# Performance work log

Measured on AMD Instinct MI355X. Metric: run time of the kernel, lower is better.

## Reference

```python
import jax, jax.numpy as jnp
import numpy as np

L = 512       # seq_len (capped by hard-coded max_length=512)
LEN = 2048    # input feature dim ('length')
D = 2048      # d_model
H = 16        # num_heads
DH = D // H   # d_head = 128
FF = 8192     # FFN hidden
EPS = 1e-5


def _pos_encoding(n, d):
    # Matches PositionalEncoderLayer buffer construction exactly.
    pos = jnp.arange(n, dtype=jnp.float32)[:, None]                              # [n,1]
    freqs = 1.0 / (2.0 * jnp.pi) / (10000.0 * jnp.exp(jnp.arange(0, d, 2, dtype=jnp.float32) / d))
    pe = jnp.zeros((n, d), dtype=jnp.float32)
    pe = pe.at[:, 0::2].set(jnp.sin(2.0 * jnp.pi * freqs * pos))
    pe = pe.at[:, 1::2].set(jnp.cos(2.0 * jnp.pi * freqs * pos))
    return pe


def _layernorm(x, g, b):
    mu = jnp.mean(x, axis=-1, keepdims=True)
    var = jnp.mean((x - mu) ** 2, axis=-1, keepdims=True)
    return (x - mu) / jnp.sqrt(var + EPS) * g + b


def setup_inputs() -> dict:
    key = jax.random.key(0)
    ks = jax.random.split(key, 12)
    def lin(k, fin, fout):
        kw, kb = jax.random.split(k)
        W = jax.random.normal(kw, (fin, fout), jnp.float32) / np.sqrt(fin)
        b = jax.random.normal(kb, (fout,), jnp.float32) * 0.01
        return W, b
    emb_W, emb_b = lin(ks[0], LEN, D)
    Wq, bq = lin(ks[1], D, D)
    Wk, bk = lin(ks[2], D, D)
    Wv, bv = lin(ks[3], D, D)
    Wo, bo = lin(ks[4], D, D)
    W1, b1 = lin(ks[5], D, FF)
    W2, b2 = lin(ks[6], FF, D)
    return {
        "sequence": jax.random.normal(ks[7], (L, LEN), jnp.float32),
        "emb_W": emb_W, "emb_b": emb_b,
        "Wq": Wq, "bq": bq, "Wk": Wk, "bk": bk, "Wv": Wv, "bv": bv,
        "Wo": Wo, "bo": bo,
        "ln_g": jnp.ones((D,), jnp.float32), "ln_b": jnp.zeros((D,), jnp.float32),
        "W1": W1, "b1": b1, "W2": W2, "b2": b2,
    }


def reference(sequence, emb_W, emb_b, Wq, bq, Wk, bk, Wv, bv, Wo, bo, ln_g, ln_b, W1, b1, W2, b2):
    # Embedding + positional encoding
    X = sequence @ emb_W + emb_b                         # [L, D]
    X = X + _pos_encoding(X.shape[0], X.shape[1])
    # Multi-head attention (keeps the module's [L, d_head, H] layout)
    Q = (X @ Wq + bq).reshape(-1, DH, H)
    K = (X @ Wk + bk).reshape(-1, DH, H)
    V = (X @ Wv + bv).reshape(-1, DH, H)
    scores = jnp.einsum('ldh,mdh->lmh', Q, K) / jnp.sqrt(jnp.float32(D))  # [L, L, H]
    attn = jax.nn.softmax(scores, axis=1)                # softmax over keys
    A = jnp.einsum('lmh,mdh->ldh', attn, V).reshape(-1, D) @ Wo + bo
    # Residual + shared LayerNorm, FFN, residual + shared LayerNorm
    Xa = _layernorm(A + X, ln_g, ln_b)
    F = jax.nn.gelu(Xa @ W1 + b1) @ W2 + b2
    return _layernorm(F + Xa, ln_g, ln_b)
```

## Files before the change

kernel.cpp:

```cpp
#include <hip/hip_runtime.h>
#include <hip/hip_bf16.h>


typedef __bf16 bf16_t;
typedef __bf16 bf16x8 __attribute__((ext_vector_type(8)));
typedef float  f32x4  __attribute__((ext_vector_type(4)));

#define SEQL 512
#define DM   2048
#define FFH  8192
#define NH   16
#define DHD  128
#define PST  ((size_t)SEQL*DM)

__device__ __forceinline__ unsigned short bfbits(float f){
  bf16_t h = (bf16_t)f;
  return __builtin_bit_cast(unsigned short, h);
}
__device__ __forceinline__ unsigned int pack2(float a, float b){
  return (unsigned int)bfbits(a) | ((unsigned int)bfbits(b) << 16);
}

__device__ __forceinline__ void gll16(const bf16_t* g, bf16_t* l){
  __builtin_amdgcn_global_load_lds(
      (const __attribute__((address_space(1))) void*)g,
      (__attribute__((address_space(3))) void*)l, 16, 0, 0);
}

__global__ __launch_bounds__(256)
void cvt_bf16(const float* __restrict__ in, bf16_t* __restrict__ out){
  const int i = (blockIdx.x * 256 + threadIdx.x) * 4;
  const float4 v = *(const float4*)(in + i);
  ushort4 o;
  o.x = bfbits(v.x); o.y = bfbits(v.y); o.z = bfbits(v.z); o.w = bfbits(v.w);
  *(ushort4*)(out + i) = o;
}

constexpr int E_PART = 0;
constexpr int E_QKV  = 1;
constexpr int E_FFN1 = 2;

template<int EPI, int PERM>
__global__ __launch_bounds__(256, 4)
void gemmF(const bf16_t* __restrict__ A,
           const float* __restrict__ W0p, const float* __restrict__ W1p,
           const float* __restrict__ W2p,
           const float* __restrict__ b0p, const float* __restrict__ b1p,
           const float* __restrict__ b2p,
           float* __restrict__ outF, bf16_t* __restrict__ o0,
           bf16_t* __restrict__ o1, bf16_t* __restrict__ o2,
           int nn, int Nw, int K, int Kc)
{
  __shared__ bf16_t sA[2][64*32];
  __shared__ bf16_t sB[2][128*32];
  const int tid  = threadIdx.x;
  const int lane = tid & 63, w = tid >> 6;
  const int wr4 = w >> 1, wc = w & 1;
  const int c = lane & 15, g = lane >> 4;

  const int nwg = gridDim.x, cpx = nwg >> 3;
  const int sblk = (blockIdx.x & 7) * cpx + (blockIdx.x >> 3);
  const int mt = sblk & 7, q = sblk >> 3;
  const int nt = q % nn, zt = q / nn;
  const int m0 = mt * 64, k0 = zt * Kc;

  const float* Wp = W0p; int nb0 = nt * 128;
  if constexpr (EPI == E_QKV){
    if (nt >= 32){ Wp = W2p; nb0 = (nt - 32) * 128; }
    else if (nt >= 16){ Wp = W1p; nb0 = (nt - 16) * 128; }
  }

  const int sr = tid >> 2, ss = tid & 3;
  const int scol = ((ss ^ ((sr >> 1) & 3)) << 3);
  const bf16_t* Asrc = A + (size_t)(m0 + sr) * K + k0 + scol;

  const int bn4 = tid & 31;
  const int kb  = (tid >> 5) * 4;
  const float* Bsrc = Wp + nb0 + bn4 * 4;

  int raA[2], raB[4];
#pragma unroll
  for (int m = 0; m < 2; ++m){
    const int r = wr4*32 + m*16 + c;
    raA[m] = r*32 + ((g ^ ((r >> 1) & 3)) << 3);
  }
#pragma unroll
  for (int n = 0; n < 4; ++n){
    const int r = wc*64 + n*16 + c;
    raB[n] = r*32 + ((g ^ ((r >> 2) & 3)) << 3);
  }

  f32x4 wr[4];

#define LOADW(kt) {                                                         \
    const int kk = k0 + (kt)*32 + kb;                                       \
    _Pragma("unroll")                                                       \
    for (int i = 0; i < 4; ++i){                                            \
      const int kr = kk + i;                                                \
      const int krow = PERM ? (((kr & 127) << 4) + (kr >> 7)) : kr;         \
      wr[i] = *(const f32x4*)(Bsrc + (size_t)krow * Nw);                    \
    } }

#define STAGEA(bf, kt) gll16(Asrc + (size_t)(kt)*32, &sA[bf][tid*8]);

#define WRITEB(bf) {                                                        \
    _Pragma("unroll")                                                       \
    for (int j = 0; j < 4; ++j){                                            \
      const int n = bn4*4 + j;                                              \
      const int el = n*32 + (kb ^ (((n >> 2) & 3) << 3));                   \
      uint2 v2;                                                             \
      v2.x = pack2(wr[0][j], wr[1][j]);                                     \
      v2.y = pack2(wr[2][j], wr[3][j]);                                     \
      *(uint2*)&sB[bf][el] = v2;                                            \
    } }

  f32x4 acc[2][4] = {};
  const int nk = Kc >> 5;

  LOADW(0);
  STAGEA(0, 0);
  WRITEB(0);
  __syncthreads();

  int buf = 0;
  for (int kt = 0; kt < nk; ++kt){
    const int nb = buf ^ 1;
    if (kt + 1 < nk){ LOADW(kt + 1); STAGEA(nb, kt + 1); }
    bf16x8 af[2], bq4[4];
#pragma unroll
    for (int m = 0; m < 2; ++m) af[m] = *(const bf16x8*)&sA[buf][raA[m]];
#pragma unroll
    for (int n = 0; n < 4; ++n) bq4[n] = *(const bf16x8*)&sB[buf][raB[n]];
#pragma unroll
    for (int m = 0; m < 2; ++m)
#pragma unroll
      for (int n = 0; n < 4; ++n)
        acc[m][n] = __builtin_amdgcn_mfma_f32_16x16x32_bf16(af[m], bq4[n], acc[m][n], 0,0,0);
    if (kt + 1 < nk){ WRITEB(nb); }
    __syncthreads();
    buf = nb;
  }
#undef LOADW
#undef STAGEA
#undef WRITEB

#pragma unroll
  for (int n = 0; n < 4; ++n){
    const int col = nt*128 + wc*64 + n*16 + c;
#pragma unroll
    for (int m = 0; m < 2; ++m){
      const int row0 = m0 + wr4*32 + m*16 + 4*g;
      const f32x4 a4 = acc[m][n];
      if constexpr (EPI == E_PART){
        float* dst = outF + (size_t)zt * PST;
#pragma unroll
        for (int rr = 0; rr < 4; ++rr)
          dst[(size_t)(row0+rr)*DM + col] = a4[rr];
      } else if constexpr (EPI == E_QKV){
        if (col < DM){
          const float bv = b0p[col];
#pragma unroll
          for (int rr = 0; rr < 4; ++rr)
            o0[(size_t)(row0+rr)*DM + col] = (bf16_t)(a4[rr] + bv);
        } else if (col < 2*DM){
          const int cc = col - DM;
          const float bv = b1p[cc];
#pragma unroll
          for (int rr = 0; rr < 4; ++rr)
            o1[(size_t)(row0+rr)*DM + cc] = (bf16_t)(a4[rr] + bv);
        } else {
          const int cc = col - 2*DM;
          const float bv = b2p[cc];
          const int hh = cc & 15, dd = cc >> 4;
          unsigned short us[4];
#pragma unroll
          for (int rr = 0; rr < 4; ++rr) us[rr] = bfbits(a4[rr] + bv);
          *(ushort4*)&o2[(size_t)(hh*DHD + dd)*SEQL + row0] =
              make_ushort4(us[0], us[1], us[2], us[3]);
        }
      } else if constexpr (EPI == E_FFN1){
        const float bv = b0p[col];
#pragma unroll
        for (int rr = 0; rr < 4; ++rr){
          const float v = a4[rr] + bv;
          const float z = v * (v*v*0.044715f + 1.0f) * 1.5957691216f;
          const float gg = v / (1.0f + __expf(-z));
          o0[(size_t)(row0+rr)*FFH + col] = (bf16_t)gg;
        }
      }
    }
  }
}

__global__ __launch_bounds__(256)
void permute_qk(const bf16_t* __restrict__ Qf, const bf16_t* __restrict__ Kf,
                bf16_t* __restrict__ Qhd, bf16_t* __restrict__ Khd)
{
  const int row = blockIdx.x, which = blockIdx.y, tid = threadIdx.x;
  const bf16_t* src = (which ? Kf : Qf) + (size_t)row * DM;
  bf16_t* dst = which ? Khd : Qhd;
  const int hh = tid >> 4, d0 = (tid & 15) * 8;
  unsigned short us[8];
#pragma unroll
  for (int j = 0; j < 8; ++j)
    us[j] = __builtin_bit_cast(unsigned short, src[(d0 + j)*NH + hh]);
  uint4 o;
  o.x = (unsigned)us[0] | ((unsigned)us[1] << 16);
  o.y = (unsigned)us[2] | ((unsigned)us[3] << 16);
  o.z = (unsigned)us[4] | ((unsigned)us[5] << 16);
  o.w = (unsigned)us[6] | ((unsigned)us[7] << 16);
  *(uint4*)&dst[(size_t)hh*(SEQL*DHD) + (size_t)row*DHD + d0] = o;
}

__global__ __launch_bounds__(256)
void attn_kernel(const bf16_t* __restrict__ Qh, const bf16_t* __restrict__ Kh,
                 const bf16_t* __restrict__ Vt, bf16_t* __restrict__ Aout)
{
  __shared__ bf16_t Pl[32*512];
  __shared__ float redm[4][32];
  __shared__ float reds[4][32];
  const int tid = threadIdx.x;
  const int lane = tid & 63, w = tid >> 6;
  const int c = lane & 15, g = lane >> 4;
  const int h = blockIdx.y;
  const int rb = blockIdx.x * 32;
  const bf16_t* Qb = Qh + (size_t)h * (SEQL*DHD);
  const bf16_t* Kb = Kh + (size_t)h * (SEQL*DHD);
  const bf16_t* Vb = Vt + (size_t)h * (SEQL*DHD);

  bf16x8 qf[2][4];
#pragma unroll
  for (int a = 0; a < 2; ++a)
#pragma unroll
    for (int ks = 0; ks < 4; ++ks)
      qf[a][ks] = *(const bf16x8*)(Qb + (size_t)(rb + a*16 + c)*DHD + ks*32 + g*8);

  f32x4 s[2][8] = {};
#pragma unroll
  for (int ks = 0; ks < 4; ++ks)
#pragma unroll
    for (int b = 0; b < 8; ++b){
      const bf16x8 kf = *(const bf16x8*)(Kb + (size_t)(w*128 + b*16 + c)*DHD + ks*32 + g*8);
      s[0][b] = __builtin_amdgcn_mfma_f32_16x16x32_bf16(qf[0][ks], kf, s[0][b], 0,0,0);
      s[1][b] = __builtin_amdgcn_mfma_f32_16x16x32_bf16(qf[1][ks], kf, s[1][b], 0,0,0);
    }
#pragma unroll
  for (int a = 0; a < 2; ++a)
#pragma unroll
    for (int b = 0; b < 8; ++b)
#pragma unroll
      for (int rr = 0; rr < 4; ++rr) s[a][b][rr] *= 0.022097086912079612f;

  float mx[2][4], sm[2][4], inv[2][4];
#pragma unroll
  for (int a = 0; a < 2; ++a)
#pragma unroll
    for (int rr = 0; rr < 4; ++rr){
      float m = s[a][0][rr];
#pragma unroll
      for (int b = 1; b < 8; ++b) m = fmaxf(m, s[a][b][rr]);
#pragma unroll
      for (int off = 1; off < 16; off <<= 1) m = fmaxf(m, __shfl_xor(m, off));
      mx[a][rr] = m;
    }
  if (c == 0)
#pragma unroll
    for (int a = 0; a < 2; ++a)
#pragma unroll
      for (int rr = 0; rr < 4; ++rr) redm[w][a*16 + 4*g + rr] = mx[a][rr];
  __syncthreads();
#pragma unroll
  for (int a = 0; a < 2; ++a)
#pragma unroll
    for (int rr = 0; rr < 4; ++rr){
      const int lr = a*16 + 4*g + rr;
      mx[a][rr] = fmaxf(fmaxf(redm[0][lr], redm[1][lr]), fmaxf(redm[2][lr], redm[3][lr]));
      sm[a][rr] = 0.f;
    }
#pragma unroll
  for (int a = 0; a < 2; ++a)
#pragma unroll
    for (int b = 0; b < 8; ++b)
#pragma unroll
      for (int rr = 0; rr < 4; ++rr){
        const float p = __expf(s[a][b][rr] - mx[a][rr]);
        s[a][b][rr] = p;
        sm[a][rr] += p;
      }
#pragma unroll
  for (int a = 0; a < 2; ++a)
#pragma unroll
    for (int rr = 0; rr < 4; ++rr){
#pragma unroll
      for (int off = 1; off < 16; off <<= 1) sm[a][rr] += __shfl_xor(sm[a][rr], off);
    }
  if (c == 0)
#pragma unroll
    for (int a = 0; a < 2; ++a)
#pragma unroll
      for (int rr = 0; rr < 4; ++rr) reds[w][a*16 + 4*g + rr] = sm[a][rr];
  __syncthreads();
#pragma unroll
  for (int a = 0; a < 2; ++a)
#pragma unroll
    for (int rr = 0; rr < 4; ++rr){
      const int lr = a*16 + 4*g + rr;
      inv[a][rr] = 1.0f / (reds[0][lr] + reds[1][lr] + reds[2][lr] + reds[3][lr]);
    }

#pragma unroll
  for (int a = 0; a < 2; ++a)
#pragma unroll
    for (int b = 0; b < 8; ++b)
#pragma unroll
      for (int rr = 0; rr < 4; ++rr){
        const int lr  = a*16 + 4*g + rr;
        const int key = w*128 + b*16 + c;
        const int slot = (key >> 3) ^ (lr & 7);
        Pl[lr*512 + slot*8 + (key & 7)] = (bf16_t)(s[a][b][rr] * inv[a][rr]);
      }
  __syncthreads();

  f32x4 o[2][2] = {};
  const int dw = w * 32;
#pragma unroll
  for (int kst = 0; kst < 16; ++kst){
    bf16x8 pa2[2];
#pragma unroll
    for (int a = 0; a < 2; ++a){
      const int r = a*16 + c;
      const int slot = (kst*4 + g) ^ (r & 7);
      pa2[a] = *(const bf16x8*)&Pl[r*512 + slot*8];
    }
#pragma unroll
    for (int db = 0; db < 2; ++db){
      const bf16x8 vf = *(const bf16x8*)(Vb + (size_t)(dw + db*16 + c)*SEQL + kst*32 + g*8);
      o[0][db] = __builtin_amdgcn_mfma_f32_16x16x32_bf16(pa2[0], vf, o[0][db], 0,0,0);
      o[1][db] = __builtin_amdgcn_mfma_f32_16x16x32_bf16(pa2[1], vf, o[1][db], 0,0,0);
    }
  }
#pragma unroll
  for (int a = 0; a < 2; ++a)
#pragma unroll
    for (int db = 0; db < 2; ++db)
#pragma unroll
      for (int rr = 0; rr < 4; ++rr){
        const int row  = rb + a*16 + 4*g + rr;
        const int col2 = h*DHD + dw + db*16 + c;
        Aout[(size_t)row*DM + col2] = (bf16_t)o[a][db][rr];
      }
}

__global__ __launch_bounds__(256)
void reduce_pos(const float* __restrict__ P, const float* __restrict__ bias,
                float* __restrict__ X, bf16_t* __restrict__ XB)
{
  const int row = blockIdx.x, c0 = threadIdx.x * 8;
  const size_t base = (size_t)row * DM + c0;
  float y[8];
#pragma unroll
  for (int j = 0; j < 8; ++j) y[j] = bias[c0 + j];
#pragma unroll
  for (int s = 0; s < 4; ++s){
    const float4 v0 = *(const float4*)(P + s*PST + base);
    const float4 v1 = *(const float4*)(P + s*PST + base + 4);
    y[0]+=v0.x; y[1]+=v0.y; y[2]+=v0.z; y[3]+=v0.w;
    y[4]+=v1.x; y[5]+=v1.y; y[6]+=v1.z; y[7]+=v1.w;
  }
#pragma unroll
  for (int j = 0; j < 8; ++j){
    const int col = c0 + j;
    const float fr  = 1e-4f * __expf(-(float)(col >> 1) * (1.0f/1024.0f));
    const float ang = (float)row * fr;
    y[j] += (col & 1) ? __cosf(ang) : __sinf(ang);
  }
  *(float4*)(X + base)     = make_float4(y[0], y[1], y[2], y[3]);
  *(float4*)(X + base + 4) = make_float4(y[4], y[5], y[6], y[7]);
  uint4 ob;
  ob.x = pack2(y[0], y[1]); ob.y = pack2(y[2], y[3]);
  ob.z = pack2(y[4], y[5]); ob.w = pack2(y[6], y[7]);
  *(uint4*)&XB[base] = ob;
}

template<int WB>
__global__ __launch_bounds__(256)
void reduce_ln(const float* __restrict__ P, const float* __restrict__ bias,
               const float* __restrict__ resid, const float* __restrict__ gam,
               const float* __restrict__ bet, float* __restrict__ outF,
               bf16_t* __restrict__ outB)
{
  const int row = blockIdx.x, tid = threadIdx.x, c0 = tid * 8;
  const size_t base = (size_t)row * DM + c0;
  float y[8];
  {
    const float4 r0 = *(const float4*)(resid + base);
    const float4 r1 = *(const float4*)(resid + base + 4);
    y[0]=r0.x; y[1]=r0.y; y[2]=r0.z; y[3]=r0.w;
    y[4]=r1.x; y[5]=r1.y; y[6]=r1.z; y[7]=r1.w;
  }
#pragma unroll
  for (int j = 0; j < 8; ++j) y[j] += bias[c0 + j];
#pragma unroll
  for (int s = 0; s < 4; ++s){
    const float4 v0 = *(const float4*)(P + s*PST + base);
    const float4 v1 = *(const float4*)(P + s*PST + base + 4);
    y[0]+=v0.x; y[1]+=v0.y; y[2]+=v0.z; y[3]+=v0.w;
    y[4]+=v1.x; y[5]+=v1.y; y[6]+=v1.z; y[7]+=v1.w;
  }
  float sm = 0.f, qs = 0.f;
#pragma unroll
  for (int j = 0; j < 8; ++j){ sm += y[j]; qs += y[j]*y[j]; }
#pragma unroll
  for (int off = 32; off >= 1; off >>= 1){
    sm += __shfl_xor(sm, off); qs += __shfl_xor(qs, off);
  }
  __shared__ float rs[4], rq[4];
  const int w = tid >> 6;
  if ((tid & 63) == 0){ rs[w] = sm; rq[w] = qs; }
  __syncthreads();
  sm = rs[0]+rs[1]+rs[2]+rs[3];
  qs = rq[0]+rq[1]+rq[2]+rq[3];
  const float mu   = sm * (1.0f/2048.0f);
  const float var  = qs * (1.0f/2048.0f) - mu*mu;
  const float rstd = rsqrtf(var + 1e-5f);
  const float4 g0 = *(const float4*)(gam + c0);
  const float4 g1 = *(const float4*)(gam + c0 + 4);
  const float4 b0 = *(const float4*)(bet + c0);
  const float4 b1 = *(const float4*)(bet + c0 + 4);
  float o[8];
  o[0] = (y[0]-mu)*rstd*g0.x + b0.x;  o[1] = (y[1]-mu)*rstd*g0.y + b0.y;
  o[2] = (y[2]-mu)*rstd*g0.z + b0.z;  o[3] = (y[3]-mu)*rstd*g0.w + b0.w;
  o[4] = (y[4]-mu)*rstd*g1.x + b1.x;  o[5] = (y[5]-mu)*rstd*g1.y + b1.y;
  o[6] = (y[6]-mu)*rstd*g1.z + b1.z;  o[7] = (y[7]-mu)*rstd*g1.w + b1.w;
  *(float4*)(outF + base)     = make_float4(o[0], o[1], o[2], o[3]);
  *(float4*)(outF + base + 4) = make_float4(o[4], o[5], o[6], o[7]);
  if constexpr (WB){
    uint4 ob;
    ob.x = pack2(o[0], o[1]); ob.y = pack2(o[2], o[3]);
    ob.z = pack2(o[4], o[5]); ob.w = pack2(o[6], o[7]);
    *(uint4*)&outB[base] = ob;
  }
}

extern "C" void kernel_launch(void* const* d_in, const int* in_sizes, int n_in,
                              void* d_out, int out_size, void* d_ws, size_t ws_size,
                              hipStream_t stream)
{
  const float* seq   = (const float*)d_in[0];
  const float* emb_W = (const float*)d_in[1];
  const float* emb_b = (const float*)d_in[2];
  const float* Wq = (const float*)d_in[3];  const float* bq = (const float*)d_in[4];
  const float* Wk = (const float*)d_in[5];  const float* bk = (const float*)d_in[6];
  const float* Wv = (const float*)d_in[7];  const float* bv = (const float*)d_in[8];
  const float* Wo = (const float*)d_in[9];  const float* bo = (const float*)d_in[10];
  const float* ln_g = (const float*)d_in[11]; const float* ln_b = (const float*)d_in[12];
  const float* W1 = (const float*)d_in[13]; const float* b1 = (const float*)d_in[14];
  const float* W2 = (const float*)d_in[15]; const float* b2 = (const float*)d_in[16];

  char* ws = (char*)d_ws;
  size_t off = 0;
  auto take = [&](size_t bytes) -> void* {
    void* p = ws + off;
    off += (bytes + 255) & ~(size_t)255;
    return p;
  };
  bf16_t* seqB = (bf16_t*)take((size_t)SEQL*DM*2);
  float*  X    = (float*) take((size_t)SEQL*DM*4);
  bf16_t* XB   = (bf16_t*)take((size_t)SEQL*DM*2);
  bf16_t* Qf   = (bf16_t*)take((size_t)SEQL*DM*2);
  bf16_t* Kf   = (bf16_t*)take((size_t)SEQL*DM*2);
  bf16_t* Qhd  = (bf16_t*)take((size_t)SEQL*DM*2);
  bf16_t* Khd  = (bf16_t*)take((size_t)SEQL*DM*2);
  bf16_t* Vt   = (bf16_t*)take((size_t)SEQL*DM*2);
  bf16_t* Afl  = (bf16_t*)take((size_t)SEQL*DM*2);
  float*  Pp   = (float*) take((size_t)4*SEQL*DM*4);
  float*  Xa   = (float*) take((size_t)SEQL*DM*4);
  bf16_t* XaB  = (bf16_t*)take((size_t)SEQL*DM*2);
  bf16_t* Hb   = (bf16_t*)take((size_t)SEQL*FFH*2);
  (void)ws_size; (void)in_sizes; (void)n_in; (void)out_size;

  cvt_bf16<<<dim3(SEQL*DM/1024), 256, 0, stream>>>(seq, seqB);

  gemmF<E_PART,0><<<dim3(512), 256, 0, stream>>>(seqB, emb_W, nullptr, nullptr,
      nullptr, nullptr, nullptr, Pp, nullptr, nullptr, nullptr, 16, DM, DM, 512);
  reduce_pos<<<SEQL, 256, 0, stream>>>(Pp, emb_b, X, XB);

  gemmF<E_QKV,0><<<dim3(384), 256, 0, stream>>>(XB, Wq, Wk, Wv,
      bq, bk, bv, nullptr, Qf, Kf, Vt, 48, DM, DM, DM);
  permute_qk<<<dim3(SEQL,2), 256, 0, stream>>>(Qf, Kf, Qhd, Khd);

  attn_kernel<<<dim3(16,16), 256, 0, stream>>>(Qhd, Khd, Vt, Afl);

  gemmF<E_PART,1><<<dim3(512), 256, 0, stream>>>(Afl, Wo, nullptr, nullptr,
      nullptr, nullptr, nullptr, Pp, nullptr, nullptr, nullptr, 16, DM, DM, 512);
  reduce_ln<1><<<SEQL, 256, 0, stream>>>(Pp, bo, X, ln_g, ln_b, Xa, XaB);

  gemmF<E_FFN1,0><<<dim3(512), 256, 0, stream>>>(XaB, W1, nullptr, nullptr,
      b1, nullptr, nullptr, nullptr, Hb, nullptr, nullptr, 64, FFH, DM, DM);

  gemmF<E_PART,0><<<dim3(512), 256, 0, stream>>>(Hb, W2, nullptr, nullptr,
      nullptr, nullptr, nullptr, Pp, nullptr, nullptr, nullptr, 16, DM, FFH, 2048);
  reduce_ln<0><<<SEQL, 256, 0, stream>>>(Pp, b2, Xa, ln_g, ln_b, (float*)d_out, nullptr);
}
```

Before: 262.2 us.

## Store weight tiles k-major in LDS with transpose reads, double split-K

The B tile is now staged into LDS in its natural row-major (k-major) order using 16-byte writes per thread, replacing the earlier scattered 8-byte transposed stores. The MFMA operand layout is recovered with ds_read_b64_tr_b16 transpose loads, followed by an explicit lgkmcnt wait and a scheduling barrier. In addition, the split-K factor for the embedding, Wo and W2 GEMMs goes from 4 to 8. That doubles the grid to 1024 blocks to improve occupancy, at the cost of twice the fp32 partial-sum traffic in the reduce kernels. The explicit wait and barrier may limit overlap of LDS reads with the MFMAs.

```diff
diff --git a/kernel.cpp b/kernel.cpp
--- a/kernel.cpp
+++ b/kernel.cpp
@@ -3,6 +3,7 @@
 
 
 typedef __bf16 bf16_t;
+typedef __bf16 bf16x4 __attribute__((ext_vector_type(4)));
 typedef __bf16 bf16x8 __attribute__((ext_vector_type(8)));
 typedef float  f32x4  __attribute__((ext_vector_type(4)));
 
@@ -25,6 +26,9 @@
   __builtin_amdgcn_global_load_lds(
       (const __attribute__((address_space(1))) void*)g,
       (__attribute__((address_space(3))) void*)l, 16, 0, 0);
+}
+__device__ __forceinline__ unsigned lds_off(const void* p){
+  return (unsigned)(uintptr_t)(const __attribute__((address_space(3))) void*)p;
 }
 
 __global__ __launch_bounds__(256)
@@ -60,8 +64,8 @@
 
   const int nwg = gridDim.x, cpx = nwg >> 3;
   const int sblk = (blockIdx.x & 7) * cpx + (blockIdx.x >> 3);
-  const int mt = sblk & 7, q = sblk >> 3;
-  const int nt = q % nn, zt = q / nn;
+  const int mt = sblk & 7, q2 = sblk >> 3;
+  const int nt = q2 % nn, zt = q2 / nn;
   const int m0 = mt * 64, k0 = zt * Kc;
 
   const float* Wp = W0p; int nb0 = nt * 128;
@@ -74,44 +78,45 @@
   const int scol = ((ss ^ ((sr >> 1) & 3)) << 3);
   const bf16_t* Asrc = A + (size_t)(m0 + sr) * K + k0 + scol;
 
-  const int bn4 = tid & 31;
-  const int kb  = (tid >> 5) * 4;
-  const float* Bsrc = Wp + nb0 + bn4 * 4;
-
-  int raA[2], raB[4];
+  const int sk = tid >> 4, sn8 = tid & 15;
+  const float* Wsrc = Wp + nb0 + sn8 * 8;
+  unsigned bOff[2];
+#pragma unroll
+  for (int q = 0; q < 2; ++q)
+    bOff[q] = (unsigned)((sn8 >> 1)*1024 + ((sk >> 2) + q*4)*128 + (sk & 3)*32 + (sn8 & 1)*16);
+
+  const unsigned sBbase[2] = { lds_off(&sB[0][0]), lds_off(&sB[1][0]) };
+  const unsigned trLane = (unsigned)(g*256 + c*8);
+
+  int raA[2];
 #pragma unroll
   for (int m = 0; m < 2; ++m){
     const int r = wr4*32 + m*16 + c;
     raA[m] = r*32 + ((g ^ ((r >> 1) & 3)) << 3);
   }
-#pragma unroll
-  for (int n = 0; n < 4; ++n){
-    const int r = wc*64 + n*16 + c;
-    raB[n] = r*32 + ((g ^ ((r >> 2) & 3)) << 3);
-  }
-
-  f32x4 wr[4];
+
+  f32x4 wv[2][2];
 
 #define LOADW(kt) {                                                         \
-    const int kk = k0 + (kt)*32 + kb;                                       \
     _Pragma("unroll")                                                       \
-    for (int i = 0; i < 4; ++i){                                            \
-      const int kr = kk + i;                                                \
+    for (int q = 0; q < 2; ++q){                                            \
+      const int kr = k0 + (kt)*32 + sk + q*16;                              \
       const int krow = PERM ? (((kr & 127) << 4) + (kr >> 7)) : kr;         \
-      wr[i] = *(const f32x4*)(Bsrc + (size_t)krow * Nw);                    \
+      wv[q][0] = *(const f32x4*)(Wsrc + (size_t)krow * Nw);                 \
+      wv[q][1] = *(const f32x4*)(Wsrc + (size_t)krow * Nw + 4);             \
     } }
 
 #define STAGEA(bf, kt) gll16(Asrc + (size_t)(kt)*32, &sA[bf][tid*8]);
 
 #define WRITEB(bf) {                                                        \
     _Pragma("unroll")                                                       \
-    for (int j = 0; j < 4; ++j){                                            \
-      const int n = bn4*4 + j;                                              \
-      const int el = n*32 + (kb ^ (((n >> 2) & 3) << 3));                   \
-      uint2 v2;                                                             \
-      v2.x = pack2(wr[0][j], wr[1][j]);                                     \
-      v2.y = pack2(wr[2][j], wr[3][j]);                                     \
-      *(uint2*)&sB[bf][el] = v2;                                            \
+    for (int q = 0; q < 2; ++q){                                            \
+      uint4 v;                                                              \
+      v.x = pack2(wv[q][0][0], wv[q][0][1]);                                \
+      v.y = pack2(wv[q][0][2], wv[q][0][3]);                                \
+      v.z = pack2(wv[q][1][0], wv[q][1][1]);                                \
+      v.w = pack2(wv[q][1][2], wv[q][1][3]);                                \
+      *(uint4*)((char*)&sB[bf][0] + bOff[q]) = v;                           \
     } }
 
   f32x4 acc[2][4] = {};
@@ -129,8 +134,19 @@
     bf16x8 af[2], bq4[4];
 #pragma unroll
     for (int m = 0; m < 2; ++m) af[m] = *(const bf16x8*)&sA[buf][raA[m]];
-#pragma unroll
-    for (int n = 0; n < 4; ++n) bq4[n] = *(const bf16x8*)&sB[buf][raB[n]];
+    {
+      const unsigned base = sBbase[buf] + (unsigned)(wc*4*1024) + trLane;
+#pragma unroll
+      for (int n = 0; n < 4; ++n){
+        bf16x4 r0, r1;
+        const unsigned a = base + (unsigned)(n*1024);
+        asm volatile("ds_read_b64_tr_b16 %0, %1" : "=v"(r0) : "v"(a));
+        asm volatile("ds_read_b64_tr_b16 %0, %1 offset:128" : "=v"(r1) : "v"(a));
+        bq4[n] = __builtin_shufflevector(r0, r1, 0,1,2,3,4,5,6,7);
+      }
+    }
+    asm volatile("s_waitcnt lgkmcnt(0)" ::: "memory");
+    __builtin_amdgcn_sched_barrier(0);
 #pragma unroll
     for (int m = 0; m < 2; ++m)
 #pragma unroll
@@ -351,6 +367,7 @@
       }
 }
 
+template<int S>
 __global__ __launch_bounds__(256)
 void reduce_pos(const float* __restrict__ P, const float* __restrict__ bias,
                 float* __restrict__ X, bf16_t* __restrict__ XB)
@@ -361,7 +378,7 @@
 #pragma unroll
   for (int j = 0; j < 8; ++j) y[j] = bias[c0 + j];
 #pragma unroll
-  for (int s = 0; s < 4; ++s){
+  for (int s = 0; s < S; ++s){
     const float4 v0 = *(const float4*)(P + s*PST + base);
     const float4 v1 = *(const float4*)(P + s*PST + base + 4);
     y[0]+=v0.x; y[1]+=v0.y; y[2]+=v0.z; y[3]+=v0.w;
@@ -382,7 +399,7 @@
   *(uint4*)&XB[base] = ob;
 }
 
-template<int WB>
+template<int S, int WB>
 __global__ __launch_bounds__(256)
 void reduce_ln(const float* __restrict__ P, const float* __restrict__ bias,
                const float* __restrict__ resid, const float* __restrict__ gam,
@@ -401,7 +418,7 @@
 #pragma unroll
   for (int j = 0; j < 8; ++j) y[j] += bias[c0 + j];
 #pragma unroll
-  for (int s = 0; s < 4; ++s){
+  for (int s = 0; s < S; ++s){
     const float4 v0 = *(const float4*)(P + s*PST + base);
     const float4 v1 = *(const float4*)(P + s*PST + base + 4);
     y[0]+=v0.x; y[1]+=v0.y; y[2]+=v0.z; y[3]+=v0.w;
@@ -473,7 +490,7 @@
   bf16_t* Khd  = (bf16_t*)take((size_t)SEQL*DM*2);
   bf16_t* Vt   = (bf16_t*)take((size_t)SEQL*DM*2);
   bf16_t* Afl  = (bf16_t*)take((size_t)SEQL*DM*2);
-  float*  Pp   = (float*) take((size_t)4*SEQL*DM*4);
+  float*  Pp   = (float*) take((size_t)8*SEQL*DM*4);
   float*  Xa   = (float*) take((size_t)SEQL*DM*4);
   bf16_t* XaB  = (bf16_t*)take((size_t)SEQL*DM*2);
   bf16_t* Hb   = (bf16_t*)take((size_t)SEQL*FFH*2);
@@ -481,9 +498,9 @@
 
   cvt_bf16<<<dim3(SEQL*DM/1024), 256, 0, stream>>>(seq, seqB);
 
-  gemmF<E_PART,0><<<dim3(512), 256, 0, stream>>>(seqB, emb_W, nullptr, nullptr,
-      nullptr, nullptr, nullptr, Pp, nullptr, nullptr, nullptr, 16, DM, DM, 512);
-  reduce_pos<<<SEQL, 256, 0, stream>>>(Pp, emb_b, X, XB);
+  gemmF<E_PART,0><<<dim3(1024), 256, 0, stream>>>(seqB, emb_W, nullptr, nullptr,
+      nullptr, nullptr, nullptr, Pp, nullptr, nullptr, nullptr, 16, DM, DM, 256);
+  reduce_pos<8><<<SEQL, 256, 0, stream>>>(Pp, emb_b, X, XB);
 
   gemmF<E_QKV,0><<<dim3(384), 256, 0, stream>>>(XB, Wq, Wk, Wv,
       bq, bk, bv, nullptr, Qf, Kf, Vt, 48, DM, DM, DM);
@@ -491,14 +508,14 @@
 
   attn_kernel<<<dim3(16,16), 256, 0, stream>>>(Qhd, Khd, Vt, Afl);
 
-  gemmF<E_PART,1><<<dim3(512), 256, 0, stream>>>(Afl, Wo, nullptr, nullptr,
-      nullptr, nullptr, nullptr, Pp, nullptr, nullptr, nullptr, 16, DM, DM, 512);
-  reduce_ln<1><<<SEQL, 256, 0, stream>>>(Pp, bo, X, ln_g, ln_b, Xa, XaB);
+  gemmF<E_PART,1><<<dim3(1024), 256, 0, stream>>>(Afl, Wo, nullptr, nullptr,
+      nullptr, nullptr, nullptr, Pp, nullptr, nullptr, nullptr, 16, DM, DM, 256);
+  reduce_ln<8,1><<<SEQL, 256, 0, stream>>>(Pp, bo, X, ln_g, ln_b, Xa, XaB);
 
   gemmF<E_FFN1,0><<<dim3(512), 256, 0, stream>>>(XaB, W1, nullptr, nullptr,
       b1, nullptr, nullptr, nullptr, Hb, nullptr, nullptr, 64, FFH, DM, DM);
 
-  gemmF<E_PART,0><<<dim3(512), 256, 0, stream>>>(Hb, W2, nullptr, nullptr,
-      nullptr, nullptr, nullptr, Pp, nullptr, nullptr, nullptr, 16, DM, FFH, 2048);
-  reduce_ln<0><<<SEQL, 256, 0, stream>>>(Pp, b2, Xa, ln_g, ln_b, (float*)d_out, nullptr);
-}
+  gemmF<E_PART,0><<<dim3(1024), 256, 0, stream>>>(Hb, W2, nullptr, nullptr,
+      nullptr, nullptr, nullptr, Pp, nullptr, nullptr, nullptr, 16, DM, FFH, 1024);
+  reduce_ln<8,0><<<SEQL, 256, 0, stream>>>(Pp, b2, Xa, ln_g, ln_b, (float*)d_out, nullptr);
+}
```

Result: slower. 281.6 us (+7.4%).
